# Kernel tuning notes

Hardware: AMD Instinct MI355X
Metric: run time of the kernel (lower is better)

Reference implementation:

```python
import jax, jax.numpy as jnp
import numpy as np

N = 8192
IN_F = 256
OUT_F = 64
ALPHA = 0.3  # LeakyReLU negative slope
NEG_INF = -9e15


def setup_inputs() -> dict:
    key = jax.random.key(0)
    k1, k2, k3, k4 = jax.random.split(key, 4)
    h = jax.random.normal(k1, (N, IN_F), dtype=jnp.float32)
    # sparse-ish binary adjacency with self loops (values are 0/1 floats)
    adj = (jax.random.uniform(k2, (N, N)) < 0.05).astype(jnp.float32)
    adj = jnp.maximum(adj, jnp.eye(N, dtype=jnp.float32))
    # xavier_uniform-style scales (gain=1.414)
    w_lim = 1.414 * np.sqrt(6.0 / (IN_F + OUT_F))
    a_lim = 1.414 * np.sqrt(6.0 / (2 * OUT_F + 1))
    W = jax.random.uniform(k3, (IN_F, OUT_F), minval=-w_lim, maxval=w_lim, dtype=jnp.float32)
    a = jax.random.uniform(k4, (2 * OUT_F, 1), minval=-a_lim, maxval=a_lim, dtype=jnp.float32)
    return {"h": h, "adj": adj, "W": W, "a": a}


def reference(h, adj, W, a):
    # Wh: [N, F]
    Wh = h @ W
    # Additive decomposition of the original concat-attention:
    # e_ij = leakyrelu(a[:F].Wh_i + a[F:].Wh_j)  -- identical math, no NxNx2F tensor
    src = Wh @ a[:OUT_F]      # [N, 1]
    dst = Wh @ a[OUT_F:]      # [N, 1]
    e = jax.nn.leaky_relu(src + dst.T, negative_slope=ALPHA)  # [N, N]
    e = e * adj               # faithful: original multiplies by adj before masking
    att = jnp.where(adj > 0, e, NEG_INF)
    att = jax.nn.softmax(att, axis=1)
    # dropout omitted (eval mode / deterministic reference)
    h_prime = att @ Wh        # [N, F]
    return jax.nn.elu(h_prime)
```

## Files before the change

### kernel.cpp

```cpp
#include <hip/hip_runtime.h>
#include <hip/hip_bf16.h>

#define N_NODES 8192
#define IN_F    256
#define OUT_F   64
#define ALPHA   0.3f
#define MBIAS   20.0f
#define CSPL    32
#define COLS_PER (N_NODES / CSPL)
#define BST     264

typedef unsigned short u16;
typedef unsigned int   u32;
typedef unsigned long long u64;
typedef __attribute__((ext_vector_type(8))) short bf16x8;
typedef __attribute__((ext_vector_type(4))) float f32x4;

__device__ __forceinline__ float bf2f(u32 u) { return __uint_as_float(u << 16); }
__device__ __forceinline__ u32 f2bfbits(float x) {
    u32 u = __float_as_uint(x);
    return (u + 0x7FFFu + ((u >> 16) & 1u)) >> 16;
}
__device__ __forceinline__ float lrelu(float s) { return s > 0.f ? s : ALPHA * s; }

__device__ __forceinline__ int detect_bf16(const void* adj) {
    return ((((const u32*)adj)[0] & 0xFFFFu) == 0x3F80u) ? 1 : 0;
}

template <bool BF16>
__device__ __forceinline__ float ld(const void* p, size_t idx) {
    if constexpr (BF16) return bf2f(((const u16*)p)[idx]);
    else                return ((const float*)p)[idx];
}

template <bool BF16>
__device__ __forceinline__ void wh4_impl(
    const void* __restrict__ h, const void* __restrict__ W,
    const void* __restrict__ a, float* __restrict__ src,
    float* __restrict__ dst, int i0, int lane, float* accv)
{
    float acc0 = 0.f, acc1 = 0.f, acc2 = 0.f, acc3 = 0.f;
#pragma unroll 8
    for (int k = 0; k < IN_F; ++k) {
        float wv = ld<BF16>(W, (size_t)k * OUT_F + lane);
        float h0 = ld<BF16>(h, (size_t)(i0 + 0) * IN_F + k);
        float h1 = ld<BF16>(h, (size_t)(i0 + 1) * IN_F + k);
        float h2 = ld<BF16>(h, (size_t)(i0 + 2) * IN_F + k);
        float h3 = ld<BF16>(h, (size_t)(i0 + 3) * IN_F + k);
        acc0 = fmaf(h0, wv, acc0);
        acc1 = fmaf(h1, wv, acc1);
        acc2 = fmaf(h2, wv, acc2);
        acc3 = fmaf(h3, wv, acc3);
    }
    float av = ld<BF16>(a, lane);
    float bv = ld<BF16>(a, OUT_F + lane);
    float accs[4] = {acc0, acc1, acc2, acc3};
#pragma unroll
    for (int r = 0; r < 4; ++r) {
        float ps = accs[r] * av, pd = accs[r] * bv;
#pragma unroll
        for (int off = 32; off > 0; off >>= 1) {
            ps += __shfl_xor(ps, off, 64);
            pd += __shfl_xor(pd, off, 64);
        }
        if (lane == 0) { src[i0 + r] = ps; dst[i0 + r] = pd; }
        accv[r] = accs[r];
    }
}

__global__ __launch_bounds__(256) void gat_wh_kernel(
    const void* __restrict__ h, const void* __restrict__ W,
    const void* __restrict__ a, const void* __restrict__ adj,
    u16* __restrict__ WhT, float* __restrict__ src, float* __restrict__ dst)
{
    __shared__ float accs[16][OUT_F];
    const int tid = threadIdx.x, wave = tid >> 6, lane = tid & 63;
    const int i0 = blockIdx.x * 16 + wave * 4;
    float av[4];
    if (detect_bf16(adj)) wh4_impl<true >(h, W, a, src, dst, i0, lane, av);
    else                  wh4_impl<false>(h, W, a, src, dst, i0, lane, av);
#pragma unroll
    for (int r = 0; r < 4; ++r) accs[wave * 4 + r][lane] = av[r];
    __syncthreads();
    if (tid < OUT_F) {
        u32 w[8];
#pragma unroll
        for (int e = 0; e < 8; ++e) {
            u32 lo = f2bfbits(accs[2 * e][tid]);
            u32 hi = f2bfbits(accs[2 * e + 1][tid]);
            w[e] = lo | (hi << 16);
        }
        u16* dstp = WhT + (size_t)tid * N_NODES + blockIdx.x * 16;
        *(uint4*)dstp       = *(uint4*)&w[0];
        *(uint4*)(dstp + 8) = *(uint4*)&w[4];
    }
}

__global__ __launch_bounds__(256, 4) void gat_attn_kernel(
    const void* __restrict__ adj, const u16* __restrict__ WhT,
    const float* __restrict__ src, const float* __restrict__ dst,
    float* __restrict__ O_part, float* __restrict__ l_part)
{
    __shared__ alignas(16) u16  Blds[64 * BST];
    __shared__ alignas(16) u64  Mlds[64 * 5];
    __shared__ alignas(16) float Dlds[COLS_PER];

    const int tid = threadIdx.x, wave = tid >> 6, lane = tid & 63;
    const int i0 = blockIdx.x * 64, c0 = blockIdx.y * COLS_PER;
    const int isbf = detect_bf16(adj);

    {
        const u16* wrow = WhT + (size_t)(tid >> 2) * N_NODES + c0 + (tid & 3) * 64;
        u16* bl = &Blds[(tid >> 2) * BST + (tid & 3) * 64];
#pragma unroll
        for (int q = 0; q < 8; ++q)
            *(uint4*)(bl + q * 8) = *(const uint4*)(wrow + q * 8);
    }
    Dlds[tid] = dst[c0 + tid];

    if (isbf) {
        const u16* base = (const u16*)adj;
#pragma unroll 4
        for (int rr = 0; rr < 16; ++rr) {
            const int row = wave * 16 + rr;
            const u16* p = base + (size_t)(i0 + row) * N_NODES + c0;
            u64 b0 = __ballot(p[lane]       != 0);
            u64 b1 = __ballot(p[64  + lane] != 0);
            u64 b2 = __ballot(p[128 + lane] != 0);
            u64 b3 = __ballot(p[192 + lane] != 0);
            u64 v = (lane == 0) ? b0 : (lane == 1) ? b1 : (lane == 2) ? b2 : b3;
            if (lane < 4) Mlds[row * 5 + lane] = v;
        }
    } else {
        const float* base = (const float*)adj;
#pragma unroll 4
        for (int rr = 0; rr < 16; ++rr) {
            const int row = wave * 16 + rr;
            const float* p = base + (size_t)(i0 + row) * N_NODES + c0;
            u64 b0 = __ballot(p[lane]       != 0.f);
            u64 b1 = __ballot(p[64  + lane] != 0.f);
            u64 b2 = __ballot(p[128 + lane] != 0.f);
            u64 b3 = __ballot(p[192 + lane] != 0.f);
            u64 v = (lane == 0) ? b0 : (lane == 1) ? b1 : (lane == 2) ? b2 : b3;
            if (lane < 4) Mlds[row * 5 + lane] = v;
        }
    }

    __syncthreads();

    const int mrow = lane & 15, kq = (lane >> 4) * 8;
    const int mloc = 16 * wave + mrow;
    const float srow = src[i0 + mloc];
    const float mbound = lrelu(srow + MBIAS);

    f32x4 acc[4] = {{0,0,0,0},{0,0,0,0},{0,0,0,0},{0,0,0,0}};
    float lacc = 0.f;

#pragma unroll
    for (int t = 0; t < 4; ++t) {
        const u64 mword = Mlds[mloc * 5 + t];
#pragma unroll
        for (int ks = 0; ks < 2; ++ks) {
            const u32 bits = (u32)(mword >> (ks * 32 + kq)) & 0xFFu;
            const float* dp = &Dlds[t * 64 + ks * 32 + kq];
            float4 dd0 = *(const float4*)dp;
            float4 dd1 = *(const float4*)(dp + 4);
            float dv[8] = {dd0.x,dd0.y,dd0.z,dd0.w, dd1.x,dd1.y,dd1.z,dd1.w};
            union { u32 w[4]; bf16x8 v; } pa;
#pragma unroll
            for (int e = 0; e < 4; ++e) {
                float s0 = lrelu(srow + dv[2 * e]);
                float s1 = lrelu(srow + dv[2 * e + 1]);
                float p0 = (bits & (1u << (2 * e)))     ? __expf(s0 - mbound) : 0.f;
                float p1 = (bits & (1u << (2 * e + 1))) ? __expf(s1 - mbound) : 0.f;
                u32 q0 = f2bfbits(p0), q1 = f2bfbits(p1);
                lacc += bf2f(q0) + bf2f(q1);
                pa.w[e] = q0 | (q1 << 16);
            }
#pragma unroll
            for (int nt = 0; nt < 4; ++nt) {
                bf16x8 bvf = *(bf16x8*)&Blds[(16 * nt + mrow) * BST + t * 64 + ks * 32 + kq];
                acc[nt] = __builtin_amdgcn_mfma_f32_16x16x32_bf16(pa.v, bvf, acc[nt], 0, 0, 0);
            }
        }
    }

    lacc += __shfl_xor(lacc, 16, 64);
    lacc += __shfl_xor(lacc, 32, 64);
    if (lane < 16) l_part[blockIdx.y * N_NODES + i0 + 16 * wave + lane] = lacc;

    float* Ob = O_part + (size_t)blockIdx.y * N_NODES * OUT_F;
#pragma unroll
    for (int nt = 0; nt < 4; ++nt)
#pragma unroll
        for (int reg = 0; reg < 4; ++reg) {
            int row = i0 + 16 * wave + (lane >> 4) * 4 + reg;
            int col = 16 * nt + (lane & 15);
            Ob[(size_t)row * OUT_F + col] = acc[nt][reg];
        }
}

__global__ __launch_bounds__(256) void gat_reduce_kernel(
    const float* __restrict__ O_part, const float* __restrict__ l_part,
    const void* __restrict__ adj, void* __restrict__ out)
{
    int gid = blockIdx.x * 256 + threadIdx.x;
    int i = gid >> 6;
    float O = 0.f, L = 0.f;
#pragma unroll 8
    for (int c = 0; c < CSPL; ++c) {
        O += O_part[(size_t)c * N_NODES * OUT_F + gid];
        L += l_part[c * N_NODES + i];
    }
    float hp = O / L;
    float o = hp > 0.f ? hp : expm1f(hp);
    if (detect_bf16(adj)) ((u16*)out)[gid] = (u16)f2bfbits(o);
    else                  ((float*)out)[gid] = o;
}

extern "C" void kernel_launch(void* const* d_in, const int* in_sizes, int n_in,
                              void* d_out, int out_size, void* d_ws, size_t ws_size,
                              hipStream_t stream)
{
    const void* h   = d_in[0];
    const void* adj = d_in[1];
    const void* W   = d_in[2];
    const void* a   = d_in[3];

    char* ws = (char*)d_ws;
    u16*   WhT    = (u16*)ws;
    float* src    = (float*)(ws + (1u << 20));
    float* dst    = (float*)(ws + (1u << 20) + 32768);
    float* O_part = (float*)(ws + (2u << 20));
    float* l_part = (float*)(ws + (66u << 20));

    gat_wh_kernel<<<N_NODES / 16, 256, 0, stream>>>(h, W, a, adj, WhT, src, dst);
    dim3 grid(N_NODES / 64, CSPL);
    gat_attn_kernel<<<grid, 256, 0, stream>>>(adj, WhT, src, dst, O_part, l_part);
    gat_reduce_kernel<<<N_NODES * OUT_F / 256, 256, 0, stream>>>(O_part, l_part, adj, d_out);
}
```

Before: 436.4 us.

## Cut column splits to 8 and stream WhT from global with register prefetch

The column-split count drops from 32 to 8, so each block handles 1024 adjacency columns instead of 256. This shrinks the partial-output buffers and the work in the reduction kernel. The shared-memory staging of WhT is removed; each wave now loads its B fragments straight from global memory, prefetching the next K-step into registers while the current MFMAs run. The trade-off is fewer blocks (1024 instead of 4096), less parallelism per block and uncoalesced global B loads that depend on cache, while the partial-sum traffic drops.

```diff
diff --git a/kernel.cpp b/kernel.cpp
--- a/kernel.cpp
+++ b/kernel.cpp
@@ -6,9 +6,10 @@
 #define OUT_F   64
 #define ALPHA   0.3f
 #define MBIAS   20.0f
-#define CSPL    32
+#define CSPL    8
 #define COLS_PER (N_NODES / CSPL)
-#define BST     264
+#define NTILES  (COLS_PER / 64)
+#define MST     17
 
 typedef unsigned short u16;
 typedef unsigned int   u32;
@@ -101,48 +102,46 @@
     const float* __restrict__ src, const float* __restrict__ dst,
     float* __restrict__ O_part, float* __restrict__ l_part)
 {
-    __shared__ alignas(16) u16  Blds[64 * BST];
-    __shared__ alignas(16) u64  Mlds[64 * 5];
+    __shared__ alignas(16) u64  Mlds[64 * MST];
     __shared__ alignas(16) float Dlds[COLS_PER];
 
     const int tid = threadIdx.x, wave = tid >> 6, lane = tid & 63;
     const int i0 = blockIdx.x * 64, c0 = blockIdx.y * COLS_PER;
     const int isbf = detect_bf16(adj);
 
-    {
-        const u16* wrow = WhT + (size_t)(tid >> 2) * N_NODES + c0 + (tid & 3) * 64;
-        u16* bl = &Blds[(tid >> 2) * BST + (tid & 3) * 64];
-#pragma unroll
-        for (int q = 0; q < 8; ++q)
-            *(uint4*)(bl + q * 8) = *(const uint4*)(wrow + q * 8);
-    }
-    Dlds[tid] = dst[c0 + tid];
+#pragma unroll
+    for (int q = 0; q < COLS_PER / 256; ++q)
+        Dlds[q * 256 + tid] = dst[c0 + q * 256 + tid];
 
     if (isbf) {
         const u16* base = (const u16*)adj;
-#pragma unroll 4
         for (int rr = 0; rr < 16; ++rr) {
             const int row = wave * 16 + rr;
             const u16* p = base + (size_t)(i0 + row) * N_NODES + c0;
-            u64 b0 = __ballot(p[lane]       != 0);
-            u64 b1 = __ballot(p[64  + lane] != 0);
-            u64 b2 = __ballot(p[128 + lane] != 0);
-            u64 b3 = __ballot(p[192 + lane] != 0);
-            u64 v = (lane == 0) ? b0 : (lane == 1) ? b1 : (lane == 2) ? b2 : b3;
-            if (lane < 4) Mlds[row * 5 + lane] = v;
+#pragma unroll
+            for (int g = 0; g < 4; ++g) {
+                u64 b0 = __ballot(p[(g * 4 + 0) * 64 + lane] != 0);
+                u64 b1 = __ballot(p[(g * 4 + 1) * 64 + lane] != 0);
+                u64 b2 = __ballot(p[(g * 4 + 2) * 64 + lane] != 0);
+                u64 b3 = __ballot(p[(g * 4 + 3) * 64 + lane] != 0);
+                u64 v = (lane == 0) ? b0 : (lane == 1) ? b1 : (lane == 2) ? b2 : b3;
+                if (lane < 4) Mlds[row * MST + g * 4 + lane] = v;
+            }
         }
     } else {
         const float* base = (const float*)adj;
-#pragma unroll 4
         for (int rr = 0; rr < 16; ++rr) {
             const int row = wave * 16 + rr;
             const float* p = base + (size_t)(i0 + row) * N_NODES + c0;
-            u64 b0 = __ballot(p[lane]       != 0.f);
-            u64 b1 = __ballot(p[64  + lane] != 0.f);
-            u64 b2 = __ballot(p[128 + lane] != 0.f);
-            u64 b3 = __ballot(p[192 + lane] != 0.f);
-            u64 v = (lane == 0) ? b0 : (lane == 1) ? b1 : (lane == 2) ? b2 : b3;
-            if (lane < 4) Mlds[row * 5 + lane] = v;
+#pragma unroll
+            for (int g = 0; g < 4; ++g) {
+                u64 b0 = __ballot(p[(g * 4 + 0) * 64 + lane] != 0.f);
+                u64 b1 = __ballot(p[(g * 4 + 1) * 64 + lane] != 0.f);
+                u64 b2 = __ballot(p[(g * 4 + 2) * 64 + lane] != 0.f);
+                u64 b3 = __ballot(p[(g * 4 + 3) * 64 + lane] != 0.f);
+                u64 v = (lane == 0) ? b0 : (lane == 1) ? b1 : (lane == 2) ? b2 : b3;
+                if (lane < 4) Mlds[row * MST + g * 4 + lane] = v;
+            }
         }
     }
 
@@ -153,36 +152,56 @@
     const float srow = src[i0 + mloc];
     const float mbound = lrelu(srow + MBIAS);
 
+    const u16* bbase = WhT + c0 + kq;
+    const size_t brow0 = (size_t)(mrow)      * N_NODES;
+    const size_t brow1 = (size_t)(16 + mrow) * N_NODES;
+    const size_t brow2 = (size_t)(32 + mrow) * N_NODES;
+    const size_t brow3 = (size_t)(48 + mrow) * N_NODES;
+
     f32x4 acc[4] = {{0,0,0,0},{0,0,0,0},{0,0,0,0},{0,0,0,0}};
     float lacc = 0.f;
 
-#pragma unroll
-    for (int t = 0; t < 4; ++t) {
-        const u64 mword = Mlds[mloc * 5 + t];
-#pragma unroll
-        for (int ks = 0; ks < 2; ++ks) {
-            const u32 bits = (u32)(mword >> (ks * 32 + kq)) & 0xFFu;
-            const float* dp = &Dlds[t * 64 + ks * 32 + kq];
-            float4 dd0 = *(const float4*)dp;
-            float4 dd1 = *(const float4*)(dp + 4);
-            float dv[8] = {dd0.x,dd0.y,dd0.z,dd0.w, dd1.x,dd1.y,dd1.z,dd1.w};
-            union { u32 w[4]; bf16x8 v; } pa;
-#pragma unroll
-            for (int e = 0; e < 4; ++e) {
-                float s0 = lrelu(srow + dv[2 * e]);
-                float s1 = lrelu(srow + dv[2 * e + 1]);
-                float p0 = (bits & (1u << (2 * e)))     ? __expf(s0 - mbound) : 0.f;
-                float p1 = (bits & (1u << (2 * e + 1))) ? __expf(s1 - mbound) : 0.f;
-                u32 q0 = f2bfbits(p0), q1 = f2bfbits(p1);
-                lacc += bf2f(q0) + bf2f(q1);
-                pa.w[e] = q0 | (q1 << 16);
-            }
-#pragma unroll
-            for (int nt = 0; nt < 4; ++nt) {
-                bf16x8 bvf = *(bf16x8*)&Blds[(16 * nt + mrow) * BST + t * 64 + ks * 32 + kq];
-                acc[nt] = __builtin_amdgcn_mfma_f32_16x16x32_bf16(pa.v, bvf, acc[nt], 0, 0, 0);
-            }
-        }
+    uint4 bc0 = *(const uint4*)(bbase + brow0);
+    uint4 bc1 = *(const uint4*)(bbase + brow1);
+    uint4 bc2 = *(const uint4*)(bbase + brow2);
+    uint4 bc3 = *(const uint4*)(bbase + brow3);
+
+    for (int s = 0; s < 2 * NTILES; ++s) {
+        const int t = s >> 1, ks = s & 1;
+
+        uint4 bn0, bn1, bn2, bn3;
+        if (s + 1 < 2 * NTILES) {
+            const int off = ((s + 1) >> 1) * 64 + ((s + 1) & 1) * 32;
+            bn0 = *(const uint4*)(bbase + brow0 + off);
+            bn1 = *(const uint4*)(bbase + brow1 + off);
+            bn2 = *(const uint4*)(bbase + brow2 + off);
+            bn3 = *(const uint4*)(bbase + brow3 + off);
+        }
+
+        const u64 mword = Mlds[mloc * MST + t];
+        const u32 bits = (u32)(mword >> (ks * 32 + kq)) & 0xFFu;
+        const float* dp = &Dlds[t * 64 + ks * 32 + kq];
+        float4 dd0 = *(const float4*)dp;
+        float4 dd1 = *(const float4*)(dp + 4);
+        float dv[8] = {dd0.x,dd0.y,dd0.z,dd0.w, dd1.x,dd1.y,dd1.z,dd1.w};
+        union { u32 w[4]; bf16x8 v; } pa;
+#pragma unroll
+        for (int e = 0; e < 4; ++e) {
+            float s0 = lrelu(srow + dv[2 * e]);
+            float s1 = lrelu(srow + dv[2 * e + 1]);
+            float p0 = (bits & (1u << (2 * e)))     ? __expf(s0 - mbound) : 0.f;
+            float p1 = (bits & (1u << (2 * e + 1))) ? __expf(s1 - mbound) : 0.f;
+            u32 q0 = f2bfbits(p0), q1 = f2bfbits(p1);
+            lacc += bf2f(q0) + bf2f(q1);
+            pa.w[e] = q0 | (q1 << 16);
+        }
+
+        acc[0] = __builtin_amdgcn_mfma_f32_16x16x32_bf16(pa.v, *(bf16x8*)&bc0, acc[0], 0, 0, 0);
+        acc[1] = __builtin_amdgcn_mfma_f32_16x16x32_bf16(pa.v, *(bf16x8*)&bc1, acc[1], 0, 0, 0);
+        acc[2] = __builtin_amdgcn_mfma_f32_16x16x32_bf16(pa.v, *(bf16x8*)&bc2, acc[2], 0, 0, 0);
+        acc[3] = __builtin_amdgcn_mfma_f32_16x16x32_bf16(pa.v, *(bf16x8*)&bc3, acc[3], 0, 0, 0);
+
+        bc0 = bn0; bc1 = bn1; bc2 = bn2; bc3 = bn3;
     }
 
     lacc += __shfl_xor(lacc, 16, 64);
@@ -207,7 +226,7 @@
     int gid = blockIdx.x * 256 + threadIdx.x;
     int i = gid >> 6;
     float O = 0.f, L = 0.f;
-#pragma unroll 8
+#pragma unroll
     for (int c = 0; c < CSPL; ++c) {
         O += O_part[(size_t)c * N_NODES * OUT_F + gid];
         L += l_part[c * N_NODES + i];
@@ -232,7 +251,7 @@
     float* src    = (float*)(ws + (1u << 20));
     float* dst    = (float*)(ws + (1u << 20) + 32768);
     float* O_part = (float*)(ws + (2u << 20));
-    float* l_part = (float*)(ws + (66u << 20));
+    float* l_part = (float*)(ws + (18u << 20));
 
     gat_wh_kernel<<<N_NODES / 16, 256, 0, stream>>>(h, W, a, adj, WhT, src, dst);
     dim3 grid(N_NODES / 64, CSPL);
```

Result: slower. 458.5 us (+5.0%).

## Precompute adjacency bitmask, repack Wh into MFMA fragment layout, and reduce column splits

Applied to the files above, without the earlier changes.

The adjacency-to-bitmask ballot moves out of the attention kernel into the prep kernel, which packs the whole matrix once into a global mask64 array. A new repack kernel stores Wh in per-lane MFMA B-fragment order, so the attention kernel reads B fragments straight from global memory with register double-buffering and drops the LDS staging of Wh. The column split falls from 32 to 8, so each block loops over 16 tiles. This shrinks O_part traffic and the reduce work, at the cost of fewer blocks and longer serial loops per block. An extra launch and the mask write and read round trip are added.

```diff
diff --git a/kernel.cpp b/kernel.cpp
--- a/kernel.cpp
+++ b/kernel.cpp
@@ -6,9 +6,12 @@
 #define OUT_F   64
 #define ALPHA   0.3f
 #define MBIAS   20.0f
-#define CSPL    32
+#define CSPL    8
 #define COLS_PER (N_NODES / CSPL)
-#define BST     264
+#define NTILES  (COLS_PER / 64)
+#define MST     17
+#define LDP     72
+#define WH_BLOCKS (N_NODES / 16)
 
 typedef unsigned short u16;
 typedef unsigned int   u32;
@@ -68,83 +71,110 @@
     }
 }
 
-__global__ __launch_bounds__(256) void gat_wh_kernel(
+__global__ __launch_bounds__(256) void gat_prep_kernel(
     const void* __restrict__ h, const void* __restrict__ W,
     const void* __restrict__ a, const void* __restrict__ adj,
-    u16* __restrict__ WhT, float* __restrict__ src, float* __restrict__ dst)
+    u16* __restrict__ WhT, float* __restrict__ src, float* __restrict__ dst,
+    u64* __restrict__ mask64)
 {
     __shared__ float accs[16][OUT_F];
     const int tid = threadIdx.x, wave = tid >> 6, lane = tid & 63;
-    const int i0 = blockIdx.x * 16 + wave * 4;
-    float av[4];
-    if (detect_bf16(adj)) wh4_impl<true >(h, W, a, src, dst, i0, lane, av);
-    else                  wh4_impl<false>(h, W, a, src, dst, i0, lane, av);
-#pragma unroll
-    for (int r = 0; r < 4; ++r) accs[wave * 4 + r][lane] = av[r];
+    const int isbf = detect_bf16(adj);
+
+    if (blockIdx.x < WH_BLOCKS) {
+        const int i0 = blockIdx.x * 16 + wave * 4;
+        float av[4];
+        if (isbf) wh4_impl<true >(h, W, a, src, dst, i0, lane, av);
+        else      wh4_impl<false>(h, W, a, src, dst, i0, lane, av);
+#pragma unroll
+        for (int r = 0; r < 4; ++r) accs[wave * 4 + r][lane] = av[r];
+        __syncthreads();
+        if (tid < OUT_F) {
+            u32 w[8];
+#pragma unroll
+            for (int e = 0; e < 8; ++e) {
+                u32 lo = f2bfbits(accs[2 * e][tid]);
+                u32 hi = f2bfbits(accs[2 * e + 1][tid]);
+                w[e] = lo | (hi << 16);
+            }
+            u16* dstp = WhT + (size_t)tid * N_NODES + blockIdx.x * 16;
+            *(uint4*)dstp       = *(uint4*)&w[0];
+            *(uint4*)(dstp + 8) = *(uint4*)&w[4];
+        }
+    } else {
+        const int wgid = (blockIdx.x - WH_BLOCKS) * 4 + wave;
+        const int NW   = 2048 * 4;
+        const int C    = (N_NODES / 256) * N_NODES;
+        if (isbf) {
+            const u16* base = (const u16*)adj;
+            for (int c = wgid; c < C; c += NW) {
+                const u16* p = base + (size_t)c * 256;
+                u64 b0 = __ballot(p[lane]       != 0);
+                u64 b1 = __ballot(p[64  + lane] != 0);
+                u64 b2 = __ballot(p[128 + lane] != 0);
+                u64 b3 = __ballot(p[192 + lane] != 0);
+                u64 v = (lane == 0) ? b0 : (lane == 1) ? b1 : (lane == 2) ? b2 : b3;
+                if (lane < 4) mask64[(size_t)c * 4 + lane] = v;
+            }
+        } else {
+            const float* base = (const float*)adj;
+            for (int c = wgid; c < C; c += NW) {
+                const float* p = base + (size_t)c * 256;
+                u64 b0 = __ballot(p[lane]       != 0.f);
+                u64 b1 = __ballot(p[64  + lane] != 0.f);
+                u64 b2 = __ballot(p[128 + lane] != 0.f);
+                u64 b3 = __ballot(p[192 + lane] != 0.f);
+                u64 v = (lane == 0) ? b0 : (lane == 1) ? b1 : (lane == 2) ? b2 : b3;
+                if (lane < 4) mask64[(size_t)c * 4 + lane] = v;
+            }
+        }
+    }
+}
+
+__global__ __launch_bounds__(256) void gat_repack_kernel(
+    const u16* __restrict__ WhT, u16* __restrict__ WhB)
+{
+    __shared__ alignas(16) u16 Btile[64 * LDP];
+    const int tid = threadIdx.x, wave = tid >> 6, lane = tid & 63;
+    const int T = blockIdx.x;
+
+    {
+        const int f = tid >> 2, q = tid & 3;
+        const u16* g = WhT + (size_t)f * N_NODES + T * 64 + q * 16;
+        *(uint4*)&Btile[f * LDP + q * 16]     = *(const uint4*)g;
+        *(uint4*)&Btile[f * LDP + q * 16 + 8] = *(const uint4*)(g + 8);
+    }
     __syncthreads();
-    if (tid < OUT_F) {
-        u32 w[8];
-#pragma unroll
-        for (int e = 0; e < 8; ++e) {
-            u32 lo = f2bfbits(accs[2 * e][tid]);
-            u32 hi = f2bfbits(accs[2 * e + 1][tid]);
-            w[e] = lo | (hi << 16);
-        }
-        u16* dstp = WhT + (size_t)tid * N_NODES + blockIdx.x * 16;
-        *(uint4*)dstp       = *(uint4*)&w[0];
-        *(uint4*)(dstp + 8) = *(uint4*)&w[4];
+
+    const int nt = wave, mrow = lane & 15, kq = (lane >> 4) * 8;
+#pragma unroll
+    for (int ks = 0; ks < 2; ++ks) {
+        uint4 frag = *(uint4*)&Btile[(16 * nt + mrow) * LDP + ks * 32 + kq];
+        u16* out = WhB + ((size_t)T * 8 + nt * 2 + ks) * 512 + lane * 8;
+        *(uint4*)out = frag;
     }
 }
 
 __global__ __launch_bounds__(256, 4) void gat_attn_kernel(
-    const void* __restrict__ adj, const u16* __restrict__ WhT,
+    const u64* __restrict__ mask64, const u16* __restrict__ WhB,
     const float* __restrict__ src, const float* __restrict__ dst,
     float* __restrict__ O_part, float* __restrict__ l_part)
 {
-    __shared__ alignas(16) u16  Blds[64 * BST];
-    __shared__ alignas(16) u64  Mlds[64 * 5];
+    __shared__ alignas(16) u64  Mlds[64 * MST];
     __shared__ alignas(16) float Dlds[COLS_PER];
 
     const int tid = threadIdx.x, wave = tid >> 6, lane = tid & 63;
     const int i0 = blockIdx.x * 64, c0 = blockIdx.y * COLS_PER;
-    const int isbf = detect_bf16(adj);
 
     {
-        const u16* wrow = WhT + (size_t)(tid >> 2) * N_NODES + c0 + (tid & 3) * 64;
-        u16* bl = &Blds[(tid >> 2) * BST + (tid & 3) * 64];
-#pragma unroll
-        for (int q = 0; q < 8; ++q)
-            *(uint4*)(bl + q * 8) = *(const uint4*)(wrow + q * 8);
-    }
-    Dlds[tid] = dst[c0 + tid];
-
-    if (isbf) {
-        const u16* base = (const u16*)adj;
-#pragma unroll 4
-        for (int rr = 0; rr < 16; ++rr) {
-            const int row = wave * 16 + rr;
-            const u16* p = base + (size_t)(i0 + row) * N_NODES + c0;
-            u64 b0 = __ballot(p[lane]       != 0);
-            u64 b1 = __ballot(p[64  + lane] != 0);
-            u64 b2 = __ballot(p[128 + lane] != 0);
-            u64 b3 = __ballot(p[192 + lane] != 0);
-            u64 v = (lane == 0) ? b0 : (lane == 1) ? b1 : (lane == 2) ? b2 : b3;
-            if (lane < 4) Mlds[row * 5 + lane] = v;
-        }
-    } else {
-        const float* base = (const float*)adj;
-#pragma unroll 4
-        for (int rr = 0; rr < 16; ++rr) {
-            const int row = wave * 16 + rr;
-            const float* p = base + (size_t)(i0 + row) * N_NODES + c0;
-            u64 b0 = __ballot(p[lane]       != 0.f);
-            u64 b1 = __ballot(p[64  + lane] != 0.f);
-            u64 b2 = __ballot(p[128 + lane] != 0.f);
-            u64 b3 = __ballot(p[192 + lane] != 0.f);
-            u64 v = (lane == 0) ? b0 : (lane == 1) ? b1 : (lane == 2) ? b2 : b3;
-            if (lane < 4) Mlds[row * 5 + lane] = v;
-        }
-    }
+        const int r = tid >> 2, q = tid & 3;
+        const u64* g = mask64 + (size_t)(i0 + r) * (N_NODES / 64) + (c0 >> 6) + q * 4;
+        *(uint4*)&Mlds[r * MST + q * 4]     = *(const uint4*)g;
+        *(uint4*)&Mlds[r * MST + q * 4 + 2] = *(const uint4*)(g + 2);
+    }
+#pragma unroll
+    for (int q = 0; q < COLS_PER / 256; ++q)
+        Dlds[q * 256 + tid] = dst[c0 + q * 256 + tid];
 
     __syncthreads();
 
@@ -153,36 +183,52 @@
     const float srow = src[i0 + mloc];
     const float mbound = lrelu(srow + MBIAS);
 
+    const u16* fb = WhB + (size_t)(blockIdx.y * NTILES) * 4096 + lane * 8;
+
     f32x4 acc[4] = {{0,0,0,0},{0,0,0,0},{0,0,0,0},{0,0,0,0}};
     float lacc = 0.f;
 
-#pragma unroll
-    for (int t = 0; t < 4; ++t) {
-        const u64 mword = Mlds[mloc * 5 + t];
-#pragma unroll
-        for (int ks = 0; ks < 2; ++ks) {
-            const u32 bits = (u32)(mword >> (ks * 32 + kq)) & 0xFFu;
-            const float* dp = &Dlds[t * 64 + ks * 32 + kq];
-            float4 dd0 = *(const float4*)dp;
-            float4 dd1 = *(const float4*)(dp + 4);
-            float dv[8] = {dd0.x,dd0.y,dd0.z,dd0.w, dd1.x,dd1.y,dd1.z,dd1.w};
-            union { u32 w[4]; bf16x8 v; } pa;
-#pragma unroll
-            for (int e = 0; e < 4; ++e) {
-                float s0 = lrelu(srow + dv[2 * e]);
-                float s1 = lrelu(srow + dv[2 * e + 1]);
-                float p0 = (bits & (1u << (2 * e)))     ? __expf(s0 - mbound) : 0.f;
-                float p1 = (bits & (1u << (2 * e + 1))) ? __expf(s1 - mbound) : 0.f;
-                u32 q0 = f2bfbits(p0), q1 = f2bfbits(p1);
-                lacc += bf2f(q0) + bf2f(q1);
-                pa.w[e] = q0 | (q1 << 16);
-            }
-#pragma unroll
-            for (int nt = 0; nt < 4; ++nt) {
-                bf16x8 bvf = *(bf16x8*)&Blds[(16 * nt + mrow) * BST + t * 64 + ks * 32 + kq];
-                acc[nt] = __builtin_amdgcn_mfma_f32_16x16x32_bf16(pa.v, bvf, acc[nt], 0, 0, 0);
-            }
-        }
+    uint4 bc0 = *(const uint4*)(fb);
+    uint4 bc1 = *(const uint4*)(fb + 1024);
+    uint4 bc2 = *(const uint4*)(fb + 2048);
+    uint4 bc3 = *(const uint4*)(fb + 3072);
+
+    for (int s = 0; s < 2 * NTILES; ++s) {
+        const int t = s >> 1, ks = s & 1;
+
+        uint4 bn0, bn1, bn2, bn3;
+        if (s + 1 < 2 * NTILES) {
+            const int off = ((s + 1) >> 1) * 4096 + ((s + 1) & 1) * 512;
+            bn0 = *(const uint4*)(fb + off);
+            bn1 = *(const uint4*)(fb + off + 1024);
+            bn2 = *(const uint4*)(fb + off + 2048);
+            bn3 = *(const uint4*)(fb + off + 3072);
+        }
+
+        const u64 mword = Mlds[mloc * MST + t];
+        const u32 bits = (u32)(mword >> (ks * 32 + kq)) & 0xFFu;
+        const float* dp = &Dlds[t * 64 + ks * 32 + kq];
+        float4 dd0 = *(const float4*)dp;
+        float4 dd1 = *(const float4*)(dp + 4);
+        float dv[8] = {dd0.x,dd0.y,dd0.z,dd0.w, dd1.x,dd1.y,dd1.z,dd1.w};
+        union { u32 w[4]; bf16x8 v; } pa;
+#pragma unroll
+        for (int e = 0; e < 4; ++e) {
+            float s0 = lrelu(srow + dv[2 * e]);
+            float s1 = lrelu(srow + dv[2 * e + 1]);
+            float p0 = (bits & (1u << (2 * e)))     ? __expf(s0 - mbound) : 0.f;
+            float p1 = (bits & (1u << (2 * e + 1))) ? __expf(s1 - mbound) : 0.f;
+            u32 q0 = f2bfbits(p0), q1 = f2bfbits(p1);
+            lacc += bf2f(q0) + bf2f(q1);
+            pa.w[e] = q0 | (q1 << 16);
+        }
+
+        acc[0] = __builtin_amdgcn_mfma_f32_16x16x32_bf16(pa.v, *(bf16x8*)&bc0, acc[0], 0, 0, 0);
+        acc[1] = __builtin_amdgcn_mfma_f32_16x16x32_bf16(pa.v, *(bf16x8*)&bc1, acc[1], 0, 0, 0);
+        acc[2] = __builtin_amdgcn_mfma_f32_16x16x32_bf16(pa.v, *(bf16x8*)&bc2, acc[2], 0, 0, 0);
+        acc[3] = __builtin_amdgcn_mfma_f32_16x16x32_bf16(pa.v, *(bf16x8*)&bc3, acc[3], 0, 0, 0);
+
+        bc0 = bn0; bc1 = bn1; bc2 = bn2; bc3 = bn3;
     }
 
     lacc += __shfl_xor(lacc, 16, 64);
@@ -207,7 +253,7 @@
     int gid = blockIdx.x * 256 + threadIdx.x;
     int i = gid >> 6;
     float O = 0.f, L = 0.f;
-#pragma unroll 8
+#pragma unroll
     for (int c = 0; c < CSPL; ++c) {
         O += O_part[(size_t)c * N_NODES * OUT_F + gid];
         L += l_part[c * N_NODES + i];
@@ -229,13 +275,16 @@
 
     char* ws = (char*)d_ws;
     u16*   WhT    = (u16*)ws;
-    float* src    = (float*)(ws + (1u << 20));
-    float* dst    = (float*)(ws + (1u << 20) + 32768);
-    float* O_part = (float*)(ws + (2u << 20));
-    float* l_part = (float*)(ws + (66u << 20));
-
-    gat_wh_kernel<<<N_NODES / 16, 256, 0, stream>>>(h, W, a, adj, WhT, src, dst);
+    u16*   WhB    = (u16*)(ws + (1u << 20));
+    float* src    = (float*)(ws + (2u << 20));
+    float* dst    = (float*)(ws + (2u << 20) + 32768);
+    u64*   mask64 = (u64*)  (ws + (3u << 20));
+    float* O_part = (float*)(ws + (16u << 20));
+    float* l_part = (float*)(ws + (32u << 20));
+
+    gat_prep_kernel<<<WH_BLOCKS + 2048, 256, 0, stream>>>(h, W, a, adj, WhT, src, dst, mask64);
+    gat_repack_kernel<<<N_NODES / 64, 256, 0, stream>>>(WhT, WhB);
     dim3 grid(N_NODES / 64, CSPL);
-    gat_attn_kernel<<<grid, 256, 0, stream>>>(adj, WhT, src, dst, O_part, l_part);
+    gat_attn_kernel<<<grid, 256, 0, stream>>>(mask64, WhB, src, dst, O_part, l_part);
     gat_reduce_kernel<<<N_NODES * OUT_F / 256, 256, 0, stream>>>(O_part, l_part, adj, d_out);
 }
```

Measured after the change: 424.4 us. 2.8% less time.
